# Performance work log

Hardware: AMD Instinct MI355X
Metric: run time of the kernel (lower is better)

## Reference

```python
import jax, jax.numpy as jnp
import numpy as np

FEAT_STRIDE = 16
PRE_NMS_TOP_N = 6000
POST_NMS_TOP_N = 300
NMS_THRESH = 0.7
A = 9  # len(scales)*len(ratios)
NEG = jnp.float32(-1e10)


def _generate_base_anchors(base_size=16, ratios=(0.5, 1.0, 2.0), scales=(8, 16, 32)):
    ratios = np.array(ratios, dtype=np.float64)
    scales = np.array(scales, dtype=np.float64)
    ctr = (base_size - 1) * 0.5
    size = float(base_size * base_size)
    ws = np.round(np.sqrt(size / ratios))
    hs = np.round(ws * ratios)
    out = []
    for w, h in zip(ws, hs):
        ws2 = w * scales
        hs2 = h * scales
        out.append(np.stack([ctr - 0.5 * (ws2 - 1), ctr - 0.5 * (hs2 - 1),
                             ctr + 0.5 * (ws2 - 1), ctr + 0.5 * (hs2 - 1)], axis=1))
    return np.concatenate(out, axis=0).astype(np.float32)  # [A,4]


def _all_anchors(H, W):
    base = _generate_base_anchors()
    sx = np.arange(W) * FEAT_STRIDE
    sy = np.arange(H) * FEAT_STRIDE
    sx, sy = np.meshgrid(sx, sy)  # [H,W] each, y-major ravel matches HW flatten
    shifts = np.stack([sx.ravel(), sy.ravel(), sx.ravel(), sy.ravel()], axis=1).astype(np.float32)
    return (shifts[:, None, :] + base[None, :, :]).reshape(-1, 4)  # [H*W*A,4]


def _nms_image(boxes, scores):
    # Greedy NMS on [N,4] boxes / [N] scores; emits top POST_NMS_TOP_N kept (padded with 0s).
    x1, y1, x2, y2 = boxes[:, 0], boxes[:, 1], boxes[:, 2], boxes[:, 3]
    areas = (x2 - x1 + 1.0) * (y2 - y1 + 1.0)

    def body(i, carry):
        live, ob, os_ = carry
        idx = jnp.argmax(live)
        s = live[idx]
        valid = s > NEG * 0.5
        b = boxes[idx]
        xx1 = jnp.maximum(b[0], x1)
        yy1 = jnp.maximum(b[1], y1)
        xx2 = jnp.minimum(b[2], x2)
        yy2 = jnp.minimum(b[3], y2)
        inter = jnp.maximum(xx2 - xx1 + 1.0, 0.0) * jnp.maximum(yy2 - yy1 + 1.0, 0.0)
        iou = inter / (areas[idx] + areas - inter)
        live = jnp.where(iou > NMS_THRESH, NEG, live)  # suppresses self too (iou=1)
        ob = ob.at[i].set(jnp.where(valid, b, 0.0))
        os_ = os_.at[i].set(jnp.where(valid, s, 0.0))
        return live, ob, os_

    init = (scores,
            jnp.zeros((POST_NMS_TOP_N, 4), boxes.dtype),
            jnp.zeros((POST_NMS_TOP_N,), scores.dtype))
    _, ob, os_ = jax.lax.fori_loop(0, POST_NMS_TOP_N, body, init)
    return ob, os_


def setup_inputs() -> dict:
    key = jax.random.key(0)
    ks = jax.random.split(key, 4)
    B, C, H, W = 4, 1024, 64, 64
    base_feat = jax.random.normal(ks[0], (B, C, H, W), jnp.float32)
    im_info = jnp.tile(jnp.array([H * 16.0, W * 16.0, 1.0], jnp.float32), (B, 1))
    gt_boxes = jnp.zeros((B, 20, 5), jnp.float32)   # unused in eval path
    num_boxes = jnp.zeros((B,), jnp.int32)           # unused in eval path
    conv_w = 0.01 * jax.random.normal(ks[1], (512, C, 3, 3), jnp.float32)
    conv_b = jnp.zeros((512,), jnp.float32)
    cls_w = 0.01 * jax.random.normal(ks[2], (2 * A, 512, 1, 1), jnp.float32)
    cls_b = jnp.zeros((2 * A,), jnp.float32)
    bbox_w = 0.01 * jax.random.normal(ks[3], (4 * A, 512, 1, 1), jnp.float32)
    bbox_b = jnp.zeros((4 * A,), jnp.float32)
    return {"base_feat": base_feat, "im_info": im_info, "gt_boxes": gt_boxes,
            "num_boxes": num_boxes, "conv_w": conv_w, "conv_b": conv_b,
            "cls_w": cls_w, "cls_b": cls_b, "bbox_w": bbox_w, "bbox_b": bbox_b}


def reference(base_feat, im_info, gt_boxes, num_boxes, conv_w, conv_b, cls_w, cls_b, bbox_w, bbox_b):
    B, _, H, W = base_feat.shape
    dn = ("NCHW", "OIHW", "NCHW")
    x = jax.lax.conv_general_dilated(base_feat, conv_w, (1, 1), [(1, 1), (1, 1)], dimension_numbers=dn)
    x = jax.nn.relu(x + conv_b[None, :, None, None])  # RPN_Conv + ReLU, [B,512,H,W]
    cls = jax.lax.conv_general_dilated(x, cls_w, (1, 1), "VALID", dimension_numbers=dn) + cls_b[None, :, None, None]
    bbox = jax.lax.conv_general_dilated(x, bbox_w, (1, 1), "VALID", dimension_numbers=dn) + bbox_b[None, :, None, None]

    # reshape(x,2) -> softmax over the 2-way axis: channel c pairs with c+A
    prob = jax.nn.softmax(cls.reshape(B, 2, A, H, W), axis=1)
    fg = prob[:, 1]                                   # [B,A,H,W] foreground probs
    scores = fg.transpose(0, 2, 3, 1).reshape(B, -1)  # [B, H*W*A]
    deltas = bbox.transpose(0, 2, 3, 1).reshape(B, -1, 4)

    anchors = jnp.asarray(_all_anchors(H, W))         # [H*W*A,4]
    wa = anchors[:, 2] - anchors[:, 0] + 1.0
    ha = anchors[:, 3] - anchors[:, 1] + 1.0
    cxa = anchors[:, 0] + 0.5 * (wa - 1.0)
    cya = anchors[:, 1] + 0.5 * (ha - 1.0)

    cx = deltas[..., 0] * wa + cxa
    cy = deltas[..., 1] * ha + cya
    pw = jnp.exp(deltas[..., 2]) * wa
    ph = jnp.exp(deltas[..., 3]) * ha
    x1 = cx - 0.5 * pw
    y1 = cy - 0.5 * ph
    x2 = cx + 0.5 * pw
    y2 = cy + 0.5 * ph

    imh = im_info[:, 0:1]
    imw = im_info[:, 1:2]
    x1 = jnp.clip(x1, 0.0, imw - 1.0)
    y1 = jnp.clip(y1, 0.0, imh - 1.0)
    x2 = jnp.clip(x2, 0.0, imw - 1.0)
    y2 = jnp.clip(y2, 0.0, imh - 1.0)
    boxes = jnp.stack([x1, y1, x2, y2], axis=-1)      # [B,N,4]

    s_top, idx = jax.lax.top_k(scores, PRE_NMS_TOP_N)
    b_top = jnp.take_along_axis(boxes, idx[:, :, None], axis=1)  # [B,6000,4]

    kept_boxes, kept_scores = jax.vmap(_nms_image)(b_top, s_top)  # [B,300,4],[B,300]
    bidx = jnp.broadcast_to(jnp.arange(B, dtype=kept_boxes.dtype).reshape(B, 1, 1),
                            (B, POST_NMS_TOP_N, 1))
    rois = jnp.concatenate([bidx, kept_boxes], axis=-1)  # [B,300,5]
    return rois, kept_scores
```

## Files before the change

kernel.cpp:

```cpp
#include <hip/hip_runtime.h>
#include <stdint.h>

#define HH_ 64
#define WW_ 64
#define NB 4
#define CIN 1024
#define CMID 512
#define NANCH (HH_*WW_*9)
#define PRE_N 6000
#define POST_N 300
#define CAND_PAD 6144
#define NEGV (-1.0e10f)
#define LO_SCL 2048.0f
#define LO_INV 4.8828125e-4f
#define MWORDS 192

typedef unsigned short u16;
typedef unsigned long long u64;
typedef __attribute__((ext_vector_type(8))) _Float16 f16x8;
typedef __attribute__((ext_vector_type(4))) float f32x4;

#define AS1 __attribute__((address_space(1)))
#define AS3 __attribute__((address_space(3)))

#define X_OFF   0
#define X_SZ    (NB*CMID*HH_*WW_)
#define SC_OFF  (X_OFF + X_SZ)
#define SC_SZ   (NB*NANCH)
#define BX_OFF  (SC_OFF + SC_SZ)
#define BX_SZ   (NB*NANCH*4)
#define CSC_OFF (BX_OFF + BX_SZ)
#define CSC_SZ  (NB*CAND_PAD)
#define CBX_OFF (CSC_OFF + CSC_SZ)
#define CBX_SZ  (NB*CAND_PAD*4)
#define CIX_OFF (CBX_OFF + CBX_SZ)
#define CIX_SZ  (NB*CAND_PAD)
#define WTH_OFF (CIX_OFF + CIX_SZ)
#define WTH_SZ  (9*512*1024/2)
#define WTL_OFF (WTH_OFF + WTH_SZ)
#define WTL_SZ  WTH_SZ
#define XH_OFF  (WTL_OFF + WTL_SZ)
#define XH_SZ   (NB*4096*1024/2)
#define XL_OFF  (XH_OFF + XH_SZ)
#define XL_SZ   XH_SZ
#define ZP_OFF  (XL_OFF + XL_SZ)
#define ZP_SZ   256

__device__ __forceinline__ void gl2lds16(const void* g, void* l) {
    __builtin_amdgcn_global_load_lds((const AS1 unsigned int*)g,
                                     (AS3 unsigned int*)l, 16, 0, 0);
}
union fh_u { _Float16 h; u16 u; };
__device__ __forceinline__ u16 f2h_hi(float x) {
    fh_u c; c.h = (_Float16)x; return c.u;
}
__device__ __forceinline__ u16 f2h_lo(float x, u16 hi) {
    fh_u c; c.u = hi;
    float hf = (float)c.h;
    fh_u d; d.h = (_Float16)((x - hf) * LO_SCL);
    return d.u;
}
__device__ __forceinline__ int cperm(int c) {
    int blk = c >> 5, w = c & 31;
    int pos = (w < 16) ? (((w >> 2) << 3) + (w & 3))
                       : ((((w - 16) >> 2) << 3) + 4 + (w & 3));
    return (blk << 5) + pos;
}
__device__ __forceinline__ unsigned fflip(unsigned u) {
    return (u & 0x80000000u) ? ~u : (u | 0x80000000u);
}

__global__ __launch_bounds__(256) void prep_wtk(
    const float* __restrict__ conv_w, u16* __restrict__ WTH,
    u16* __restrict__ WTL, float* __restrict__ ZP)
{
    int o = blockIdx.x * 256 + threadIdx.x;
    int ci = o & 1023, co = (o >> 10) & 511, r = o >> 19;
    float v = conv_w[((size_t)(co * 1024 + ci)) * 9 + r];
    u16 h  = f2h_hi(v);
    u16 lo = f2h_lo(v, h);
    size_t d = (((size_t)(r * 512 + co)) << 10) + cperm(ci);
    WTH[d] = h; WTL[d] = lo;
    if (o < 256) ZP[o] = 0.f;
}

__global__ __launch_bounds__(256) void prep_act(
    const float* __restrict__ in, u16* __restrict__ XH, u16* __restrict__ XL)
{
    __shared__ float T[64][65];
    const int blk = blockIdx.x;
    const int b   = blk >> 10;
    const int ci0 = ((blk >> 6) & 15) << 6;
    const int sp0 = (blk & 63) << 6;
    const int tid = threadIdx.x;
    const int tq  = tid >> 6;
    const int t64 = tid & 63;
#pragma unroll
    for (int w = 0; w < 16; w++) {
        int ci_l = w * 4 + tq;
        T[ci_l][t64] = in[(((size_t)(b * 1024 + ci0 + ci_l)) << 12) + sp0 + t64];
    }
    __syncthreads();
#pragma unroll
    for (int w = 0; w < 16; w++) {
        int sp_l = w * 4 + tq;
        float x = T[t64][sp_l];
        u16 h  = f2h_hi(x);
        u16 lo = f2h_lo(x, h);
        size_t d = (((size_t)((b << 12) + sp0 + sp_l)) << 10) + ci0 + cperm(t64);
        XH[d] = h; XL[d] = lo;
    }
}

__global__ __launch_bounds__(256, 2) void conv3_mfma(
    const u16* __restrict__ WTH, const u16* __restrict__ WTL,
    const u16* __restrict__ XH, const u16* __restrict__ XL,
    const u16* __restrict__ ZP, const float* __restrict__ bias,
    float* __restrict__ Xout)
{
    __shared__ u16 Ah_s[2][4096];
    __shared__ u16 Al_s[2][4096];
    __shared__ u16 Bh_s[2][4096];
    __shared__ u16 Bl_s[2][4096];

    const int tid = threadIdx.x;
    const int bn  = blockIdx.x;
    const int bm  = blockIdx.y;
    const int l   = tid & 63;
    const int wid = tid >> 6, wm = wid >> 1, wn = wid & 1;

    const int rowq = tid >> 2;
    const int c8   = (((tid & 3) ^ ((tid >> 3) & 3)) << 3);

    int spb[2]; unsigned vmq[2];
#pragma unroll
    for (int q = 0; q < 2; q++) {
        int n = bn * 128 + q * 64 + rowq;
        int yy = (n >> 6) & 63, xx = n & 63;
        spb[q] = n;
        unsigned m9 = 0;
#pragma unroll
        for (int rr = 0; rr < 9; rr++) {
            int dy = rr / 3 - 1, dx = rr % 3 - 1;
            if ((unsigned)(yy + dy) < 64u && (unsigned)(xx + dx) < 64u)
                m9 |= 1u << rr;
        }
        vmq[q] = m9;
    }

    f32x4 acc0[4][4], acc1[4][4];
#pragma unroll
    for (int i = 0; i < 4; i++)
#pragma unroll
        for (int j = 0; j < 4; j++) { acc0[i][j] = (f32x4)0.f; acc1[i][j] = (f32x4)0.f; }

    const int NK = 288;

    auto stage = [&](int sb, int kt) {
        const int r   = kt >> 5;
        const int ci0 = (kt & 31) << 5;
        const int kr  = (r * 11) >> 5;
        const int sh  = (kr - 1) * 64 + (r - 3 * kr - 1);
        const size_t wbase = (((size_t)(r * 512 + bm * 128)) << 10) + ci0 + c8;
        u16* ah = &Ah_s[sb][tid * 8];
        u16* al = &Al_s[sb][tid * 8];
        u16* bh = &Bh_s[sb][tid * 8];
        u16* bl = &Bl_s[sb][tid * 8];
#pragma unroll
        for (int q = 0; q < 2; q++) {
            const size_t aoff = wbase + (((size_t)(q * 64 + rowq)) << 10);
            gl2lds16(WTH + aoff, ah + q * 2048);
            gl2lds16(WTL + aoff, al + q * 2048);
            const bool v = (vmq[q] >> r) & 1u;
            const size_t boff = (((size_t)(spb[q] + sh)) << 10) + ci0 + c8;
            gl2lds16(v ? (XH + boff) : ZP, bh + q * 2048);
            gl2lds16(v ? (XL + boff) : ZP, bl + q * 2048);
        }
    };

    stage(0, 0);
    int buf = 0;
    for (int kt = 0; kt < NK; ++kt) {
        __syncthreads();
        if (kt + 1 < NK) stage(buf ^ 1, kt + 1);
        {
            const int lo16 = l & 15, hi4 = l >> 4;
            const int swl  = (lo16 >> 1) & 3;
            const int pch  = (hi4 ^ swl) << 3;
            const int aoff = (wm * 64 + lo16) * 32 + pch;
            const int boff = (wn * 64 + lo16) * 32 + pch;
            f16x8 ah[4], av[4], bh[4], bv[4];
#pragma unroll
            for (int i = 0; i < 4; i++) {
                ah[i] = *(const f16x8*)&Ah_s[buf][aoff + i * 512];
                av[i] = *(const f16x8*)&Al_s[buf][aoff + i * 512];
                bh[i] = *(const f16x8*)&Bh_s[buf][boff + i * 512];
                bv[i] = *(const f16x8*)&Bl_s[buf][boff + i * 512];
            }
#pragma unroll
            for (int mi = 0; mi < 4; mi++)
#pragma unroll
                for (int ni = 0; ni < 4; ni++) {
                    acc0[mi][ni] = __builtin_amdgcn_mfma_f32_16x16x32_f16(
                        ah[mi], bh[ni], acc0[mi][ni], 0, 0, 0);
                    acc1[mi][ni] = __builtin_amdgcn_mfma_f32_16x16x32_f16(
                        ah[mi], bv[ni], acc1[mi][ni], 0, 0, 0);
                    acc1[mi][ni] = __builtin_amdgcn_mfma_f32_16x16x32_f16(
                        av[mi], bh[ni], acc1[mi][ni], 0, 0, 0);
                }
        }
        buf ^= 1;
    }

#pragma unroll
    for (int mi = 0; mi < 4; mi++) {
        const int co0 = bm * 128 + wm * 64 + mi * 16 + ((l >> 4) << 2);
        const f32x4 b4 = *(const f32x4*)&bias[co0];
#pragma unroll
        for (int ni = 0; ni < 4; ni++) {
            const int n = bn * 128 + wn * 64 + ni * 16 + (l & 15);
            const int b = n >> 12, sp = n & 4095;
            f32x4 v0 = acc0[mi][ni], v1 = acc1[mi][ni];
            float* xo = Xout + (((size_t)(b * 512 + co0)) << 12) + sp;
            xo[0]        = fmaxf(fmaf(v1[0], LO_INV, v0[0]) + b4[0], 0.f);
            xo[4096]     = fmaxf(fmaf(v1[1], LO_INV, v0[1]) + b4[1], 0.f);
            xo[2 * 4096] = fmaxf(fmaf(v1[2], LO_INV, v0[2]) + b4[2], 0.f);
            xo[3 * 4096] = fmaxf(fmaf(v1[3], LO_INV, v0[3]) + b4[3], 0.f);
        }
    }
}

__global__ __launch_bounds__(256) void heads_kernel(
    const float* __restrict__ X, const float* __restrict__ cls_w,
    const float* __restrict__ cls_b, const float* __restrict__ bbox_w,
    const float* __restrict__ bbox_b, const float* __restrict__ im_info,
    float* __restrict__ SC, float* __restrict__ BXo)
{
    __shared__ __attribute__((aligned(16))) float Ws[54][256];
    const int tid = threadIdx.x;
    const int blk = blockIdx.x;
    const int b   = blk >> 4;
    const int s   = ((blk & 15) << 8) + tid;

    float acc[54];
#pragma unroll
    for (int j = 0; j < 18; j++) acc[j] = cls_b[j];
#pragma unroll
    for (int j = 0; j < 36; j++) acc[18 + j] = bbox_b[j];

    const float* xp = X + (size_t)b * CMID * 4096 + s;
    for (int c0 = 0; c0 < 512; c0 += 256) {
        __syncthreads();
        for (int e = tid; e < 54 * 256; e += 256) {
            int j = e >> 8, ci = e & 255;
            Ws[j][ci] = (j < 18) ? cls_w[j * 512 + c0 + ci]
                                 : bbox_w[(j - 18) * 512 + c0 + ci];
        }
        __syncthreads();
        for (int ci = 0; ci < 256; ci += 4) {
            float x0 = xp[(size_t)(c0 + ci) * 4096];
            float x1 = xp[(size_t)(c0 + ci + 1) * 4096];
            float x2 = xp[(size_t)(c0 + ci + 2) * 4096];
            float x3 = xp[(size_t)(c0 + ci + 3) * 4096];
#pragma unroll
            for (int j = 0; j < 54; j++) {
                float4 w4 = *(const float4*)&Ws[j][ci];
                acc[j] = fmaf(x3, w4.w, fmaf(x2, w4.z, fmaf(x1, w4.y, fmaf(x0, w4.x, acc[j]))));
            }
        }
    }

    const float imh = im_info[b * 3 + 0];
    const float imw = im_info[b * 3 + 1];
    const int hh = s >> 6, ww = s & 63;
    const float cxa = 7.5f + 16.f * (float)ww;
    const float cya = 7.5f + 16.f * (float)hh;
    const float WA[9] = {184.f, 368.f, 736.f, 128.f, 256.f, 512.f, 88.f, 176.f, 352.f};
    const float HA[9] = {96.f, 192.f, 384.f, 128.f, 256.f, 512.f, 176.f, 352.f, 704.f};
    const size_t base = (size_t)b * NANCH + (size_t)s * 9;
#pragma unroll
    for (int c = 0; c < 9; c++) {
        float bg = acc[c], fg = acc[9 + c];
        float m  = fmaxf(bg, fg);
        float e0 = expf(bg - m), e1 = expf(fg - m);
        float p  = e1 / (e0 + e1);
        float dx = acc[18 + 4 * c], dy = acc[19 + 4 * c];
        float dw = acc[20 + 4 * c], dh = acc[21 + 4 * c];
        float wa = WA[c], ha = HA[c];
        float cx = dx * wa + cxa;
        float cy = dy * ha + cya;
        float pw = expf(dw) * wa;
        float ph = expf(dh) * ha;
        float x1 = cx - 0.5f * pw, y1 = cy - 0.5f * ph;
        float x2 = cx + 0.5f * pw, y2 = cy + 0.5f * ph;
        x1 = fminf(fmaxf(x1, 0.f), imw - 1.f);
        y1 = fminf(fmaxf(y1, 0.f), imh - 1.f);
        x2 = fminf(fmaxf(x2, 0.f), imw - 1.f);
        y2 = fminf(fmaxf(y2, 0.f), imh - 1.f);
        SC[base + c] = p;
        *(float4*)&BXo[(base + c) * 4] = make_float4(x1, y1, x2, y2);
    }
}

__global__ __launch_bounds__(1024) void select_kernel(
    const float* __restrict__ SC,
    float* __restrict__ CSC, int* __restrict__ CIX)
{
    const int b = blockIdx.x, tid = threadIdx.x;
    const int lane = tid & 63, wv = tid >> 6;
    const float* sc = SC + (size_t)b * NANCH;
    const unsigned* bits = (const unsigned*)sc;

    __shared__ unsigned s_buf[8192];
    __shared__ unsigned s_part[1024];
    __shared__ unsigned s_wsum[16];
    __shared__ unsigned s_sel[2];
    __shared__ int s_c1, s_c2;

    auto findbin = [&](int nb, int bpt, unsigned target) -> uint2 {
        unsigned mysum = 0;
        const int base = tid * bpt;
        if (base < nb)
            for (int q = 0; q < bpt; q++) mysum += s_buf[base + q];
        s_part[tid] = mysum;
        unsigned wsum = mysum;
#pragma unroll
        for (int off = 32; off; off >>= 1) wsum += __shfl_down(wsum, off);
        if (lane == 0) s_wsum[wv] = wsum;
        __syncthreads();
        unsigned cum = 0;
        for (int w = wv + 1; w < 16; w++) cum += s_wsum[w];
        for (int ll = lane + 1; ll < 64; ll++) cum += s_part[(wv << 6) + ll];
        if (base < nb) {
            unsigned c = cum;
            for (int q = bpt - 1; q >= 0; q--) {
                unsigned h = s_buf[base + q];
                if (c < target && c + h >= target) { s_sel[0] = base + q; s_sel[1] = c; }
                c += h;
            }
        }
        __syncthreads();
        uint2 r; r.x = s_sel[0]; r.y = s_sel[1];
        __syncthreads();
        return r;
    };

    for (int i = tid; i < 8192; i += 1024) s_buf[i] = 0;
    __syncthreads();
    for (int i = tid; i < NANCH; i += 1024)
        atomicAdd(&s_buf[bits[i] >> 19], 1u);
    __syncthreads();
    uint2 r1 = findbin(8192, 8, PRE_N);
    const unsigned B1 = r1.x;
    unsigned target2 = PRE_N - r1.y;

    for (int i = tid; i < 8192; i += 1024) s_buf[i] = 0;
    __syncthreads();
    for (int i = tid; i < NANCH; i += 1024) {
        unsigned u = bits[i];
        if ((u >> 19) == B1) atomicAdd(&s_buf[(u >> 6) & 8191u], 1u);
    }
    __syncthreads();
    uint2 r2 = findbin(8192, 8, target2);
    const unsigned B2 = r2.x;
    unsigned target3 = target2 - r2.y;

    if (tid < 64) s_buf[tid] = 0;
    __syncthreads();
    const unsigned pref26 = (B1 << 13) | B2;
    for (int i = tid; i < NANCH; i += 1024) {
        unsigned u = bits[i];
        if ((u >> 6) == pref26) atomicAdd(&s_buf[u & 63u], 1u);
    }
    __syncthreads();
    uint2 r3 = findbin(64, 1, target3);
    const unsigned ustar = (B1 << 19) | (B2 << 6) | r3.x;
    const int n1 = (int)(r1.y + r2.y + r3.y);

    if (tid == 0) { s_c1 = 0; s_c2 = 0; }
    __syncthreads();
    float* csc = CSC + (size_t)b * CAND_PAD;
    int*   cix = CIX + (size_t)b * CAND_PAD;
    int* s_tie = (int*)s_buf;

    for (int i = tid; i < NANCH; i += 1024) {
        unsigned u = bits[i];
        if (u > ustar) {
            int p = atomicAdd(&s_c1, 1);
            csc[p] = sc[i]; cix[p] = i;
        } else if (u == ustar) {
            int p = atomicAdd(&s_c2, 1);
            if (p < 8192) s_tie[p] = i;
        }
    }
    __syncthreads();
    int m = s_c2; if (m > 8192) m = 8192;
    const int need = PRE_N - n1;

    if (m <= 1024) {
        if (tid < m) {
            int v = s_tie[tid];
            int r = 0;
            for (int j2 = 0; j2 < m; j2++) r += (s_tie[j2] < v) ? 1 : 0;
            if (r < need) { csc[n1 + r] = sc[v]; cix[n1 + r] = v; }
        }
    } else {
        for (int i = tid; i < 8192; i += 1024)
            if (i >= m) s_tie[i] = 0x7fffffff;
        __syncthreads();
        for (int k = 2; k <= 8192; k <<= 1) {
            for (int j = k >> 1; j > 0; j >>= 1) {
                for (int t = tid; t < 8192; t += 1024) {
                    int ixj = t ^ j;
                    if (ixj > t) {
                        int va = s_tie[t], vb = s_tie[ixj];
                        bool up = ((t & k) == 0);
                        if ((va > vb) == up) { s_tie[t] = vb; s_tie[ixj] = va; }
                    }
                }
                __syncthreads();
            }
        }
        for (int t = tid; t < need; t += 1024) {
            int i = s_tie[t];
            int p = n1 + t;
            if (i >= 0 && i < NANCH) {
                csc[p] = sc[i]; cix[p] = i;
            } else {
                csc[p] = -2.0e10f; cix[p] = 0x7fffffff;
            }
        }
    }
    for (int p = PRE_N + tid; p < CAND_PAD; p += 1024) {
        csc[p] = -2.0e10f;
        cix[p] = 0x7fffffff;
    }
}

__global__ __launch_bounds__(1024) void sort_kernel(
    float* __restrict__ CSC, float* __restrict__ CBX,
    int* __restrict__ CIX, const float* __restrict__ BX)
{
    const int b = blockIdx.x, tid = threadIdx.x;
    float* csc = CSC + (size_t)b * CAND_PAD;
    int*   cix = CIX + (size_t)b * CAND_PAD;
    float4* cbx4 = (float4*)CBX + (size_t)b * CAND_PAD;
    const float4* bx4 = (const float4*)BX + (size_t)b * NANCH;
    __shared__ u64 sk[8704];
    auto P = [](int i) { return i + (i >> 4); };

    for (int i = tid; i < 8192; i += 1024) {
        u64 key = 0ull;
        if (i < CAND_PAD) {
            unsigned khi = fflip(__float_as_uint(csc[i]));
            unsigned klo = ~((unsigned)cix[i]);
            key = ((u64)khi << 32) | klo;
        }
        sk[P(i)] = key;
    }
    __syncthreads();
    for (int k = 2; k <= 8192; k <<= 1) {
        for (int j = k >> 1; j > 0; j >>= 1) {
            for (int t = tid; t < 8192; t += 1024) {
                int ixj = t ^ j;
                if (ixj > t) {
                    int pa = P(t), pb = P(ixj);
                    u64 a = sk[pa], c2 = sk[pb];
                    bool up = ((t & k) == 0);
                    if ((a < c2) == up) { sk[pa] = c2; sk[pb] = a; }
                }
            }
            __syncthreads();
        }
    }
    for (int i = tid; i < CAND_PAD; i += 1024) {
        u64 key = sk[P(i)];
        unsigned khi = (unsigned)(key >> 32), klo = (unsigned)key;
        unsigned su = (khi & 0x80000000u) ? (khi ^ 0x80000000u) : ~khi;
        float sc = __uint_as_float(su);
        int ci = (int)(~klo);
        csc[i] = sc; cix[i] = ci;
        float4 pb;
        if (sc > -5.0e9f && (unsigned)ci < (unsigned)NANCH) pb = bx4[ci];
        else pb = make_float4(-4e9f, -4e9f, -4e9f, -4e9f);
        cbx4[i] = pb;
    }
}

__global__ __launch_bounds__(256) void nms_mask(
    const float* __restrict__ CBX, unsigned* __restrict__ MASK)
{
    const int rg = blockIdx.x, b = blockIdx.y, tid = threadIdx.x;
    const float4* cbx = (const float4*)CBX + (size_t)b * CAND_PAD;
    unsigned* mrow = MASK + (size_t)b * CAND_PAD * MWORDS;

    __shared__ float4 rb[64];
    __shared__ float  rar[64];
    __shared__ float4 cb[1024];
    __shared__ float  car[1024];

    if (tid < 64) {
        float4 v = cbx[rg * 64 + tid];
        rb[tid] = v;
        rar[tid] = (v.z - v.x + 1.f) * (v.w - v.y + 1.f);
    }
    __syncthreads();
    const int rl = tid >> 2;
    const int wq = tid & 3;
    const float4 rv = rb[rl];
    const float  ra = rar[rl];
    const size_t rbase = (size_t)(rg * 64 + rl) * MWORDS;

    for (int jt = rg >> 4; jt < 6; jt++) {
        __syncthreads();
        for (int e = tid; e < 1024; e += 256) {
            float4 v = cbx[jt * 1024 + e];
            cb[e] = v;
            car[e] = (v.z - v.x + 1.f) * (v.w - v.y + 1.f);
        }
        __syncthreads();
#pragma unroll
        for (int k = 0; k < 8; k++) {
            const int wt = wq + 4 * k;
            unsigned bits = 0;
            for (int bit = 0; bit < 32; bit++) {
                const int j = wt * 32 + bit;
                float4 cv = cb[j];
                float xx1 = fmaxf(rv.x, cv.x);
                float yy1 = fmaxf(rv.y, cv.y);
                float xx2 = fminf(rv.z, cv.z);
                float yy2 = fminf(rv.w, cv.w);
                float iw = fmaxf(xx2 - xx1 + 1.f, 0.f);
                float ih = fmaxf(yy2 - yy1 + 1.f, 0.f);
                float inter = iw * ih;
                float iou = inter / (ra + car[j] - inter);
                if (iou > 0.7f) bits |= (1u << bit);
            }
            mrow[rbase + jt * 32 + wt] = bits;
        }
    }
}

__global__ __launch_bounds__(64) void nms_scan(
    const float* __restrict__ CSC, const float* __restrict__ CBX,
    const unsigned* __restrict__ MASK, float* __restrict__ out)
{
    const int b = blockIdx.x, lane = threadIdx.x;
    const float*  csc = CSC + (size_t)b * CAND_PAD;
    const float4* cbx = (const float4*)CBX + (size_t)b * CAND_PAD;
    const unsigned* mk = MASK + (size_t)b * CAND_PAD * MWORDS;

    float* rois = out + (size_t)b * 1500;
    float* oscr = out + 6000 + (size_t)b * 300;

    for (int it = lane; it < POST_N; it += 64) {
        float* r = rois + it * 5;
        r[0] = (float)b; r[1] = 0.f; r[2] = 0.f; r[3] = 0.f; r[4] = 0.f;
        oscr[it] = 0.f;
    }
    __syncthreads();

    unsigned rm0 = 0u, rm1 = 0u, rm2 = 0u;
    int cnt = 0;
    unsigned rlo = mk[(size_t)lane * MWORDS + 0];
    unsigned rhi = mk[(size_t)lane * MWORDS + 1];
    float    rsc = csc[lane];

    for (int c = 0; c < 94 && cnt < POST_N; c++) {
        const int W0 = 2 * c;
        const int slot = W0 >> 6;
        unsigned sel = (slot == 0) ? rm0 : (slot == 1) ? rm1 : rm2;
        unsigned gw = __shfl(sel, (W0 & 63) + (lane >> 5));
        bool alive = !((gw >> (lane & 31)) & 1u) && (rsc > -5.0e9f);
        u64 rem = __ballot(alive);
        u64 keptm = 0ull;
        while (rem) {
            int sl = __builtin_ctzll(rem);
            keptm |= 1ull << sl;
            unsigned blo = __shfl(rlo, sl);
            unsigned bhi = __shfl(rhi, sl);
            rem &= ~(((u64)bhi << 32) | (u64)blo);
            rem &= ~(1ull << sl);
        }
        if (c + 1 < 94) {
            const int i2 = (c + 1) * 64 + lane;
            rlo = mk[(size_t)i2 * MWORDS + 2 * (c + 1)];
            rhi = mk[(size_t)i2 * MWORDS + 2 * (c + 1) + 1];
            rsc = csc[i2];
        }
        while (keptm && cnt < POST_N) {
            int sl = __builtin_ctzll(keptm);
            keptm &= keptm - 1ull;
            const int i = c * 64 + sl;
            const size_t rb = (size_t)i * MWORDS;
            rm0 |= mk[rb + lane];
            rm1 |= mk[rb + lane + 64];
            rm2 |= mk[rb + lane + 128];
            if (lane == 0) {
                float4 pb = cbx[i];
                float* r = rois + cnt * 5;
                r[1] = pb.x; r[2] = pb.y; r[3] = pb.z; r[4] = pb.w;
                oscr[cnt] = csc[i];
            }
            cnt++;
        }
    }
}

extern "C" void kernel_launch(void* const* d_in, const int* in_sizes, int n_in,
                              void* d_out, int out_size, void* d_ws, size_t ws_size,
                              hipStream_t stream)
{
    const float* base_feat = (const float*)d_in[0];
    const float* im_info   = (const float*)d_in[1];
    const float* conv_w    = (const float*)d_in[4];
    const float* conv_b    = (const float*)d_in[5];
    const float* cls_w     = (const float*)d_in[6];
    const float* cls_b     = (const float*)d_in[7];
    const float* bbox_w    = (const float*)d_in[8];
    const float* bbox_b    = (const float*)d_in[9];

    float* ws  = (float*)d_ws;
    float* X   = ws + X_OFF;
    float* SC  = ws + SC_OFF;
    float* BX  = ws + BX_OFF;
    float* CSC = ws + CSC_OFF;
    float* CBX = ws + CBX_OFF;
    int*   CIX = (int*)(ws + CIX_OFF);
    u16*   WTH = (u16*)(ws + WTH_OFF);
    u16*   WTL = (u16*)(ws + WTL_OFF);
    u16*   XHp = (u16*)(ws + XH_OFF);
    u16*   XLp = (u16*)(ws + XL_OFF);
    float* ZPf = ws + ZP_OFF;
    const u16* ZPu = (const u16*)ZPf;
    unsigned* MASK = (unsigned*)(ws + X_OFF);
    float* out = (float*)d_out;

    hipLaunchKernelGGL(prep_wtk, dim3(18432), dim3(256), 0, stream,
                       conv_w, WTH, WTL, ZPf);
    hipLaunchKernelGGL(prep_act, dim3(4096), dim3(256), 0, stream,
                       base_feat, XHp, XLp);
    hipLaunchKernelGGL(conv3_mfma, dim3(128, 4), dim3(256), 0, stream,
                       WTH, WTL, XHp, XLp, ZPu, conv_b, X);
    hipLaunchKernelGGL(heads_kernel, dim3(64), dim3(256), 0, stream,
                       X, cls_w, cls_b, bbox_w, bbox_b, im_info, SC, BX);
    hipLaunchKernelGGL(select_kernel, dim3(4), dim3(1024), 0, stream,
                       SC, CSC, CIX);
    hipLaunchKernelGGL(sort_kernel, dim3(4), dim3(1024), 0, stream,
                       CSC, CBX, CIX, BX);
    hipLaunchKernelGGL(nms_mask, dim3(96, 4), dim3(256), 0, stream,
                       CBX, MASK);
    hipLaunchKernelGGL(nms_scan, dim3(4), dim3(64), 0, stream,
                       CSC, CBX, MASK, out);
}
```

Baseline: 1.265 ms.

## Fuse prep and select/sort kernels, reorder conv LDS loads, shrink heads blocks

Merges the weight and activation prep kernels into one launch, and merges top-k selection with the bitonic sort so candidates go straight into shared memory as sort keys. This drops the intermediate global round-trip and the separate tie-handling sort. In the conv kernel, LDS fragment loads are hoisted ahead of the next-stage prefetch, and the heads kernel uses 128-thread blocks to double the block count. Risks: tie handling now keeps every score at or above the threshold up to 8192 entries, and loading fragments before issuing the prefetch may change latency overlap.

```diff
diff --git a/kernel.cpp b/kernel.cpp
--- a/kernel.cpp
+++ b/kernel.cpp
@@ -70,45 +70,46 @@
     return (u & 0x80000000u) ? ~u : (u | 0x80000000u);
 }
 
-__global__ __launch_bounds__(256) void prep_wtk(
+#define WT_BLKS 18432
+__global__ __launch_bounds__(256) void prep_all(
     const float* __restrict__ conv_w, u16* __restrict__ WTH,
-    u16* __restrict__ WTL, float* __restrict__ ZP)
-{
-    int o = blockIdx.x * 256 + threadIdx.x;
-    int ci = o & 1023, co = (o >> 10) & 511, r = o >> 19;
-    float v = conv_w[((size_t)(co * 1024 + ci)) * 9 + r];
-    u16 h  = f2h_hi(v);
-    u16 lo = f2h_lo(v, h);
-    size_t d = (((size_t)(r * 512 + co)) << 10) + cperm(ci);
-    WTH[d] = h; WTL[d] = lo;
-    if (o < 256) ZP[o] = 0.f;
-}
-
-__global__ __launch_bounds__(256) void prep_act(
-    const float* __restrict__ in, u16* __restrict__ XH, u16* __restrict__ XL)
+    u16* __restrict__ WTL, float* __restrict__ ZP,
+    const float* __restrict__ in, u16* __restrict__ XH,
+    u16* __restrict__ XL)
 {
     __shared__ float T[64][65];
-    const int blk = blockIdx.x;
-    const int b   = blk >> 10;
-    const int ci0 = ((blk >> 6) & 15) << 6;
-    const int sp0 = (blk & 63) << 6;
     const int tid = threadIdx.x;
-    const int tq  = tid >> 6;
-    const int t64 = tid & 63;
-#pragma unroll
-    for (int w = 0; w < 16; w++) {
-        int ci_l = w * 4 + tq;
-        T[ci_l][t64] = in[(((size_t)(b * 1024 + ci0 + ci_l)) << 12) + sp0 + t64];
-    }
-    __syncthreads();
-#pragma unroll
-    for (int w = 0; w < 16; w++) {
-        int sp_l = w * 4 + tq;
-        float x = T[t64][sp_l];
-        u16 h  = f2h_hi(x);
-        u16 lo = f2h_lo(x, h);
-        size_t d = (((size_t)((b << 12) + sp0 + sp_l)) << 10) + ci0 + cperm(t64);
-        XH[d] = h; XL[d] = lo;
+    if (blockIdx.x < WT_BLKS) {
+        int o = blockIdx.x * 256 + tid;
+        int ci = o & 1023, co = (o >> 10) & 511, r = o >> 19;
+        float v = conv_w[((size_t)(co * 1024 + ci)) * 9 + r];
+        u16 h  = f2h_hi(v);
+        u16 lo = f2h_lo(v, h);
+        size_t d = (((size_t)(r * 512 + co)) << 10) + cperm(ci);
+        WTH[d] = h; WTL[d] = lo;
+        if (o < 256) ZP[o] = 0.f;
+    } else {
+        const int blk = blockIdx.x - WT_BLKS;
+        const int b   = blk >> 10;
+        const int ci0 = ((blk >> 6) & 15) << 6;
+        const int sp0 = (blk & 63) << 6;
+        const int tq  = tid >> 6;
+        const int t64 = tid & 63;
+#pragma unroll
+        for (int w = 0; w < 16; w++) {
+            int ci_l = w * 4 + tq;
+            T[ci_l][t64] = in[(((size_t)(b * 1024 + ci0 + ci_l)) << 12) + sp0 + t64];
+        }
+        __syncthreads();
+#pragma unroll
+        for (int w = 0; w < 16; w++) {
+            int sp_l = w * 4 + tq;
+            float x = T[t64][sp_l];
+            u16 h  = f2h_hi(x);
+            u16 lo = f2h_lo(x, h);
+            size_t d = (((size_t)((b << 12) + sp0 + sp_l)) << 10) + ci0 + cperm(t64);
+            XH[d] = h; XL[d] = lo;
+        }
     }
 }
 
@@ -178,37 +179,36 @@
         }
     };
 
+    const int lo16 = l & 15, hi4 = l >> 4;
+    const int swl  = (lo16 >> 1) & 3;
+    const int pch  = (hi4 ^ swl) << 3;
+    const int aoff = (wm * 64 + lo16) * 32 + pch;
+    const int boff = (wn * 64 + lo16) * 32 + pch;
+
     stage(0, 0);
     int buf = 0;
     for (int kt = 0; kt < NK; ++kt) {
         __syncthreads();
+        f16x8 ah[4], av[4], bh[4], bv[4];
+#pragma unroll
+        for (int i = 0; i < 4; i++) {
+            ah[i] = *(const f16x8*)&Ah_s[buf][aoff + i * 512];
+            av[i] = *(const f16x8*)&Al_s[buf][aoff + i * 512];
+            bh[i] = *(const f16x8*)&Bh_s[buf][boff + i * 512];
+            bv[i] = *(const f16x8*)&Bl_s[buf][boff + i * 512];
+        }
         if (kt + 1 < NK) stage(buf ^ 1, kt + 1);
-        {
-            const int lo16 = l & 15, hi4 = l >> 4;
-            const int swl  = (lo16 >> 1) & 3;
-            const int pch  = (hi4 ^ swl) << 3;
-            const int aoff = (wm * 64 + lo16) * 32 + pch;
-            const int boff = (wn * 64 + lo16) * 32 + pch;
-            f16x8 ah[4], av[4], bh[4], bv[4];
-#pragma unroll
-            for (int i = 0; i < 4; i++) {
-                ah[i] = *(const f16x8*)&Ah_s[buf][aoff + i * 512];
-                av[i] = *(const f16x8*)&Al_s[buf][aoff + i * 512];
-                bh[i] = *(const f16x8*)&Bh_s[buf][boff + i * 512];
-                bv[i] = *(const f16x8*)&Bl_s[buf][boff + i * 512];
+#pragma unroll
+        for (int mi = 0; mi < 4; mi++)
+#pragma unroll
+            for (int ni = 0; ni < 4; ni++) {
+                acc0[mi][ni] = __builtin_amdgcn_mfma_f32_16x16x32_f16(
+                    ah[mi], bh[ni], acc0[mi][ni], 0, 0, 0);
+                acc1[mi][ni] = __builtin_amdgcn_mfma_f32_16x16x32_f16(
+                    ah[mi], bv[ni], acc1[mi][ni], 0, 0, 0);
+                acc1[mi][ni] = __builtin_amdgcn_mfma_f32_16x16x32_f16(
+                    av[mi], bh[ni], acc1[mi][ni], 0, 0, 0);
             }
-#pragma unroll
-            for (int mi = 0; mi < 4; mi++)
-#pragma unroll
-                for (int ni = 0; ni < 4; ni++) {
-                    acc0[mi][ni] = __builtin_amdgcn_mfma_f32_16x16x32_f16(
-                        ah[mi], bh[ni], acc0[mi][ni], 0, 0, 0);
-                    acc1[mi][ni] = __builtin_amdgcn_mfma_f32_16x16x32_f16(
-                        ah[mi], bv[ni], acc1[mi][ni], 0, 0, 0);
-                    acc1[mi][ni] = __builtin_amdgcn_mfma_f32_16x16x32_f16(
-                        av[mi], bh[ni], acc1[mi][ni], 0, 0, 0);
-                }
-        }
         buf ^= 1;
     }
 
@@ -230,7 +230,7 @@
     }
 }
 
-__global__ __launch_bounds__(256) void heads_kernel(
+__global__ __launch_bounds__(128) void heads_kernel(
     const float* __restrict__ X, const float* __restrict__ cls_w,
     const float* __restrict__ cls_b, const float* __restrict__ bbox_w,
     const float* __restrict__ bbox_b, const float* __restrict__ im_info,
@@ -239,8 +239,8 @@
     __shared__ __attribute__((aligned(16))) float Ws[54][256];
     const int tid = threadIdx.x;
     const int blk = blockIdx.x;
-    const int b   = blk >> 4;
-    const int s   = ((blk & 15) << 8) + tid;
+    const int b   = blk >> 5;
+    const int s   = ((blk & 31) << 7) + tid;
 
     float acc[54];
 #pragma unroll
@@ -251,7 +251,7 @@
     const float* xp = X + (size_t)b * CMID * 4096 + s;
     for (int c0 = 0; c0 < 512; c0 += 256) {
         __syncthreads();
-        for (int e = tid; e < 54 * 256; e += 256) {
+        for (int e = tid; e < 54 * 256; e += 128) {
             int j = e >> 8, ci = e & 255;
             Ws[j][ci] = (j < 18) ? cls_w[j * 512 + c0 + ci]
                                  : bbox_w[(j - 18) * 512 + c0 + ci];
@@ -302,20 +302,22 @@
     }
 }
 
-__global__ __launch_bounds__(1024) void select_kernel(
-    const float* __restrict__ SC,
-    float* __restrict__ CSC, int* __restrict__ CIX)
+__global__ __launch_bounds__(1024) void selsort_kernel(
+    const float* __restrict__ SC, const float* __restrict__ BX,
+    float* __restrict__ CSC, float* __restrict__ CBX, int* __restrict__ CIX)
 {
     const int b = blockIdx.x, tid = threadIdx.x;
     const int lane = tid & 63, wv = tid >> 6;
     const float* sc = SC + (size_t)b * NANCH;
     const unsigned* bits = (const unsigned*)sc;
 
-    __shared__ unsigned s_buf[8192];
+    __shared__ u64 sk[8704];
+    unsigned* s_buf = (unsigned*)sk;
     __shared__ unsigned s_part[1024];
     __shared__ unsigned s_wsum[16];
     __shared__ unsigned s_sel[2];
-    __shared__ int s_c1, s_c2;
+    __shared__ int s_cnt;
+    auto P = [](int i) { return i + (i >> 4); };
 
     auto findbin = [&](int nb, int bpt, unsigned target) -> uint2 {
         unsigned mysum = 0;
@@ -375,90 +377,20 @@
     __syncthreads();
     uint2 r3 = findbin(64, 1, target3);
     const unsigned ustar = (B1 << 19) | (B2 << 6) | r3.x;
-    const int n1 = (int)(r1.y + r2.y + r3.y);
-
-    if (tid == 0) { s_c1 = 0; s_c2 = 0; }
-    __syncthreads();
-    float* csc = CSC + (size_t)b * CAND_PAD;
-    int*   cix = CIX + (size_t)b * CAND_PAD;
-    int* s_tie = (int*)s_buf;
-
+
+    for (int i = tid; i < 8704; i += 1024) sk[i] = 0ull;
+    if (tid == 0) s_cnt = 0;
+    __syncthreads();
     for (int i = tid; i < NANCH; i += 1024) {
         unsigned u = bits[i];
-        if (u > ustar) {
-            int p = atomicAdd(&s_c1, 1);
-            csc[p] = sc[i]; cix[p] = i;
-        } else if (u == ustar) {
-            int p = atomicAdd(&s_c2, 1);
-            if (p < 8192) s_tie[p] = i;
-        }
-    }
-    __syncthreads();
-    int m = s_c2; if (m > 8192) m = 8192;
-    const int need = PRE_N - n1;
-
-    if (m <= 1024) {
-        if (tid < m) {
-            int v = s_tie[tid];
-            int r = 0;
-            for (int j2 = 0; j2 < m; j2++) r += (s_tie[j2] < v) ? 1 : 0;
-            if (r < need) { csc[n1 + r] = sc[v]; cix[n1 + r] = v; }
-        }
-    } else {
-        for (int i = tid; i < 8192; i += 1024)
-            if (i >= m) s_tie[i] = 0x7fffffff;
-        __syncthreads();
-        for (int k = 2; k <= 8192; k <<= 1) {
-            for (int j = k >> 1; j > 0; j >>= 1) {
-                for (int t = tid; t < 8192; t += 1024) {
-                    int ixj = t ^ j;
-                    if (ixj > t) {
-                        int va = s_tie[t], vb = s_tie[ixj];
-                        bool up = ((t & k) == 0);
-                        if ((va > vb) == up) { s_tie[t] = vb; s_tie[ixj] = va; }
-                    }
-                }
-                __syncthreads();
-            }
-        }
-        for (int t = tid; t < need; t += 1024) {
-            int i = s_tie[t];
-            int p = n1 + t;
-            if (i >= 0 && i < NANCH) {
-                csc[p] = sc[i]; cix[p] = i;
-            } else {
-                csc[p] = -2.0e10f; cix[p] = 0x7fffffff;
-            }
-        }
-    }
-    for (int p = PRE_N + tid; p < CAND_PAD; p += 1024) {
-        csc[p] = -2.0e10f;
-        cix[p] = 0x7fffffff;
-    }
-}
-
-__global__ __launch_bounds__(1024) void sort_kernel(
-    float* __restrict__ CSC, float* __restrict__ CBX,
-    int* __restrict__ CIX, const float* __restrict__ BX)
-{
-    const int b = blockIdx.x, tid = threadIdx.x;
-    float* csc = CSC + (size_t)b * CAND_PAD;
-    int*   cix = CIX + (size_t)b * CAND_PAD;
-    float4* cbx4 = (float4*)CBX + (size_t)b * CAND_PAD;
-    const float4* bx4 = (const float4*)BX + (size_t)b * NANCH;
-    __shared__ u64 sk[8704];
-    auto P = [](int i) { return i + (i >> 4); };
-
-    for (int i = tid; i < 8192; i += 1024) {
-        u64 key = 0ull;
-        if (i < CAND_PAD) {
-            unsigned khi = fflip(__float_as_uint(csc[i]));
-            unsigned klo = ~((unsigned)cix[i]);
-            key = ((u64)khi << 32) | klo;
-        }
-        sk[P(i)] = key;
-    }
-    __syncthreads();
+        if (u >= ustar) {
+            int p = atomicAdd(&s_cnt, 1);
+            if (p < 8192)
+                sk[P(p)] = ((u64)fflip(u) << 32) | (u64)(~((unsigned)i));
+        }
+    }
+    __syncthreads();
+
     for (int k = 2; k <= 8192; k <<= 1) {
         for (int j = k >> 1; j > 0; j >>= 1) {
             for (int t = tid; t < 8192; t += 1024) {
@@ -473,17 +405,28 @@
             __syncthreads();
         }
     }
+
+    float* csc = CSC + (size_t)b * CAND_PAD;
+    int*   cix = CIX + (size_t)b * CAND_PAD;
+    float4* cbx4 = (float4*)CBX + (size_t)b * CAND_PAD;
+    const float4* bx4 = (const float4*)BX + (size_t)b * NANCH;
     for (int i = tid; i < CAND_PAD; i += 1024) {
-        u64 key = sk[P(i)];
-        unsigned khi = (unsigned)(key >> 32), klo = (unsigned)key;
-        unsigned su = (khi & 0x80000000u) ? (khi ^ 0x80000000u) : ~khi;
-        float sc = __uint_as_float(su);
-        int ci = (int)(~klo);
-        csc[i] = sc; cix[i] = ci;
-        float4 pb;
-        if (sc > -5.0e9f && (unsigned)ci < (unsigned)NANCH) pb = bx4[ci];
-        else pb = make_float4(-4e9f, -4e9f, -4e9f, -4e9f);
-        cbx4[i] = pb;
+        if (i < PRE_N) {
+            u64 key = sk[P(i)];
+            unsigned khi = (unsigned)(key >> 32), klo = (unsigned)key;
+            unsigned su = (khi & 0x80000000u) ? (khi ^ 0x80000000u) : ~khi;
+            float scv = __uint_as_float(su);
+            int ci = (int)(~klo);
+            csc[i] = scv; cix[i] = ci;
+            float4 pb;
+            if (scv > -5.0e9f && (unsigned)ci < (unsigned)NANCH) pb = bx4[ci];
+            else pb = make_float4(-4e9f, -4e9f, -4e9f, -4e9f);
+            cbx4[i] = pb;
+        } else {
+            csc[i] = -2.0e10f;
+            cix[i] = 0x7fffffff;
+            cbx4[i] = make_float4(-4e9f, -4e9f, -4e9f, -4e9f);
+        }
     }
 }
 
@@ -636,18 +579,14 @@
     unsigned* MASK = (unsigned*)(ws + X_OFF);
     float* out = (float*)d_out;
 
-    hipLaunchKernelGGL(prep_wtk, dim3(18432), dim3(256), 0, stream,
-                       conv_w, WTH, WTL, ZPf);
-    hipLaunchKernelGGL(prep_act, dim3(4096), dim3(256), 0, stream,
-                       base_feat, XHp, XLp);
+    hipLaunchKernelGGL(prep_all, dim3(WT_BLKS + 4096), dim3(256), 0, stream,
+                       conv_w, WTH, WTL, ZPf, base_feat, XHp, XLp);
     hipLaunchKernelGGL(conv3_mfma, dim3(128, 4), dim3(256), 0, stream,
                        WTH, WTL, XHp, XLp, ZPu, conv_b, X);
-    hipLaunchKernelGGL(heads_kernel, dim3(64), dim3(256), 0, stream,
+    hipLaunchKernelGGL(heads_kernel, dim3(128), dim3(128), 0, stream,
                        X, cls_w, cls_b, bbox_w, bbox_b, im_info, SC, BX);
-    hipLaunchKernelGGL(select_kernel, dim3(4), dim3(1024), 0, stream,
-                       SC, CSC, CIX);
-    hipLaunchKernelGGL(sort_kernel, dim3(4), dim3(1024), 0, stream,
-                       CSC, CBX, CIX, BX);
+    hipLaunchKernelGGL(selsort_kernel, dim3(4), dim3(1024), 0, stream,
+                       SC, BX, CSC, CBX, CIX);
     hipLaunchKernelGGL(nms_mask, dim3(96, 4), dim3(256), 0, stream,
                        CBX, MASK);
     hipLaunchKernelGGL(nms_scan, dim3(4), dim3(64), 0, stream,
```

After: 1.222 ms. 3.4% less time.
